# Kernel tuning notes

Measured on AMD Instinct MI355X. Metric: run time of the kernel, lower is better.

## Reference

```python
import jax, jax.numpy as jnp
import numpy as np

NUM_EXPERTS = 4
MLP_RATIO = 4


def setup_inputs() -> dict:
    key = jax.random.key(0)
    k1, k2, k3, k4, k5, k6 = jax.random.split(key, 6)
    B, N, D = 4, 4096, 1024
    OUT = 1024
    H = D * MLP_RATIO
    x = jax.random.normal(k1, (B, N, D), dtype=jnp.float32)
    expert_mask = jax.random.randint(k2, (B, N), 0, NUM_EXPERTS, dtype=jnp.int64)
    w1 = jax.random.normal(k3, (H, D), dtype=jnp.float32) * 0.02
    b1 = jax.random.normal(k4, (H,), dtype=jnp.float32) * 0.02
    w2 = jax.random.normal(k5, (OUT, H), dtype=jnp.float32) * 0.02
    b2 = jax.random.normal(k6, (OUT,), dtype=jnp.float32) * 0.02
    return {"x": x, "expert_mask": expert_mask, "w1": w1, "b1": b1, "w2": w2, "b2": b2}


def reference(x, expert_mask, w1, b1, w2, b2):
    # x: [B, N, D]; expert_mask: [B, N] in [0, NUM_EXPERTS)
    D = x.shape[-1]
    OUT = w2.shape[0]
    E = NUM_EXPERTS
    y = jnp.zeros(x.shape[:-1] + (OUT,), dtype=x.dtype)
    for e in range(E):
        shift = E - 1 - e  # expert E-1 uses full width
        d_in = D >> shift
        d_hid = d_in * MLP_RATIO
        d_out = OUT >> shift
        # nested slice of shared weights
        h = jax.nn.gelu(
            jnp.einsum('bnd,hd->bnh', x[..., :d_in], w1[:d_hid, :d_in]) + b1[:d_hid],
            approximate=False,
        )
        ye = jnp.einsum('bnh,oh->bno', h, w2[:d_out, :d_hid]) + b2[:d_out]
        ye = jnp.pad(ye, ((0, 0), (0, 0), (0, OUT - d_out)))  # zero-fill unused dims
        y = y + jnp.where((expert_mask == e)[..., None], ye, jnp.zeros((), dtype=x.dtype))
    return y
```

## Files before the change

kernel.cpp:

```cpp
#include <hip/hip_runtime.h>
#include <hip/hip_bf16.h>

#define T_TOK 16384
#define DMODEL 1024
#define HDIM 4096
#define OUTD 1024

typedef __attribute__((ext_vector_type(8))) short short8_t;
typedef __attribute__((ext_vector_type(4))) float f32x4;

#define WS_COUNTS_OFF 0
#define WS_LIST_OFF 128
#define WS_XC_OFF   ((size_t)1 << 20)
#define WS_W1BF_OFF ((size_t)34 << 20)
#define WS_W2BF_OFF ((size_t)43 << 20)
#define WS_HBUF_OFF ((size_t)52 << 20)

#define W1N (HDIM * DMODEL)
#define W2N (OUTD * HDIM)

__device__ __forceinline__ short f2bf(float f) {
    union { float f; unsigned u; } x; x.f = f;
    unsigned r = x.u + 0x7FFFu + ((x.u >> 16) & 1u);
    return (short)(r >> 16);
}

__device__ __forceinline__ float gelu_fast(float v) {
    float z = fabsf(v) * 0.7071067811865476f;
    float t = __builtin_amdgcn_rcpf(fmaf(0.3275911f, z, 1.0f));
    float poly = t * fmaf(t, fmaf(t, fmaf(t, fmaf(t, 1.061405429f, -1.453152027f),
                                          1.421413741f), -0.284496736f),
                          0.254829592f);
    float e = fmaf(-poly, __expf(-z * z), 1.0f);
    float erfv = copysignf(e, v);
    return 0.5f * v * (1.0f + erfv);
}

__device__ __forceinline__ void conv8(const float* __restrict__ s, short* __restrict__ d) {
    const float4* s4 = (const float4*)s;
    float4 f0 = s4[0], f1 = s4[1];
    short8_t v;
    v[0] = f2bf(f0.x); v[1] = f2bf(f0.y); v[2] = f2bf(f0.z); v[3] = f2bf(f0.w);
    v[4] = f2bf(f1.x); v[5] = f2bf(f1.y); v[6] = f2bf(f1.z); v[7] = f2bf(f1.w);
    *(short8_t*)d = v;
}

__device__ __forceinline__ void gl_lds16(const short* g, short* lds) {
    __builtin_amdgcn_global_load_lds(
        (const __attribute__((address_space(1))) void*)g,
        (__attribute__((address_space(3))) void*)lds, 16, 0, 0);
}

__device__ __forceinline__ void bases_for(const int* __restrict__ counts, int e,
                                          unsigned long long* hb,
                                          unsigned long long* xb) {
    unsigned long long h = 0, x = 0;
    for (int i = 0; i < e; ++i) {
        unsigned long long c = (unsigned long long)counts[i];
        int din = 128 << i;
        x += c * (unsigned long long)din;
        h += c * (unsigned long long)(din * 4);
    }
    *hb = h; *xb = x;
}

__global__ void k_convert(const float* __restrict__ w1, const float* __restrict__ w2,
                          short* __restrict__ w1bf, short* __restrict__ w2bf,
                          int* counts) {
    if (blockIdx.x == 0 && threadIdx.x < 4) counts[threadIdx.x] = 0;
    size_t elem = ((size_t)blockIdx.x * blockDim.x + threadIdx.x) * 8;
    if (elem < (size_t)W1N) {
        conv8(w1 + elem, w1bf + elem);
    } else {
        size_t o = elem - W1N; conv8(w2 + o, w2bf + o);
    }
}

__global__ void k_build(const int* __restrict__ mask, int* counts, int* list) {
    __shared__ int hcnt[4], hb[4], hpos[4];
    int tid = threadIdx.x;
    if (tid < 4) hcnt[tid] = 0;
    __syncthreads();
    int t = blockIdx.x * 256 + tid;
    int e = mask[t] & 3;
    atomicAdd(&hcnt[e], 1);
    __syncthreads();
    if (tid < 4) { hb[tid] = atomicAdd(&counts[tid], hcnt[tid]); hpos[tid] = 0; }
    __syncthreads();
    int p = atomicAdd(&hpos[e], 1);
    list[e * T_TOK + hb[e] + p] = t;
}

__global__ void k_xgather(const float* __restrict__ x, const int* __restrict__ counts,
                          const int* __restrict__ list, short* __restrict__ xc) {
    const int e = blockIdx.y;
    const int d_in = 128 << e;
    const int cnt = counts[e];
    unsigned long long hbD, xb;
    bases_for(counts, e, &hbD, &xb);
    const size_t nel = (size_t)cnt * d_in;
    const int* lst = list + e * T_TOK;
    short* dst = xc + xb;
    for (size_t idx = ((size_t)blockIdx.x * 256 + threadIdx.x) * 8; idx < nel;
         idx += (size_t)gridDim.x * 256 * 8) {
        int row = (int)(idx >> (7 + e));
        int col = (int)(idx & (d_in - 1));
        int tok = lst[row];
        conv8(x + (size_t)tok * DMODEL + col, dst + idx);
    }
}

__global__ __launch_bounds__(256) void k_pass1(
    const short* __restrict__ xc, const short* __restrict__ w1bf,
    const float* __restrict__ b1, const int* __restrict__ counts,
    short* __restrict__ hbuf)
{
    int by = blockIdx.y;
    int e, nt;
    if (by < 32)      { e = 3; nt = by; }
    else if (by < 48) { e = 2; nt = by - 32; }
    else if (by < 56) { e = 1; nt = by - 48; }
    else              { e = 0; nt = by - 56; }
    const int d_in = 128 << e;
    const int d_hid = d_in * 4;
    const int n0 = nt * 128;
    const int cnt = counts[e];
    unsigned long long hb, xb;
    bases_for(counts, e, &hb, &xb);
    const short* xe = xc + xb;

    __shared__ short Ab[64 * 64];
    __shared__ short Bb[128 * 64];

    const int tid = threadIdx.x;
    const int lane = tid & 63;
    const int w = tid >> 6;
    const int l3 = lane >> 3;
    const int ch = lane & 7;
    const int wm = (w & 1) * 32;
    const int wn = (w >> 1) * 64;

    for (int m0 = blockIdx.x * 64; m0 < cnt; m0 += 64 * 64) {
        int rA[2];
#pragma unroll
        for (int j = 0; j < 2; ++j) {
            int rr = m0 + j * 32 + w * 8 + l3;
            rA[j] = (rr >= cnt) ? (cnt - 1) : rr;
        }

        f32x4 acc[2][4];
#pragma unroll
        for (int i = 0; i < 2; ++i)
#pragma unroll
            for (int j = 0; j < 4; ++j)
                acc[i][j] = (f32x4){0.f, 0.f, 0.f, 0.f};

        for (int k0 = 0; k0 < d_in; k0 += 64) {
#pragma unroll
            for (int j = 0; j < 2; ++j) {
                int r = j * 32 + w * 8 + l3;
                gl_lds16(xe + (size_t)rA[j] * d_in + k0 + ((ch ^ (r & 7)) << 3),
                         &Ab[(j * 32 + w * 8) * 64]);
            }
#pragma unroll
            for (int j = 0; j < 4; ++j) {
                int r = j * 32 + w * 8 + l3;
                gl_lds16(w1bf + (size_t)(n0 + r) * DMODEL + k0 + ((ch ^ (r & 7)) << 3),
                         &Bb[(j * 32 + w * 8) * 64]);
            }
            __syncthreads();
#pragma unroll
            for (int kk = 0; kk < 2; ++kk) {
                short8_t af[2], bfr[4];
                const int q = (lane >> 4) + kk * 4;
#pragma unroll
                for (int mt = 0; mt < 2; ++mt) {
                    int row = wm + mt * 16 + (lane & 15);
                    af[mt] = *(const short8_t*)&Ab[((row << 3) | (q ^ (row & 7))) << 3];
                }
#pragma unroll
                for (int ntn = 0; ntn < 4; ++ntn) {
                    int row = wn + ntn * 16 + (lane & 15);
                    bfr[ntn] = *(const short8_t*)&Bb[((row << 3) | (q ^ (row & 7))) << 3];
                }
#pragma unroll
                for (int mt = 0; mt < 2; ++mt)
#pragma unroll
                    for (int ntn = 0; ntn < 4; ++ntn)
                        acc[mt][ntn] = __builtin_amdgcn_mfma_f32_16x16x32_bf16(
                            af[mt], bfr[ntn], acc[mt][ntn], 0, 0, 0);
            }
            __syncthreads();
        }

        const int cl = lane & 15;
        const int qr = lane >> 4;
#pragma unroll
        for (int ntn = 0; ntn < 4; ++ntn) {
            int col = n0 + wn + ntn * 16 + cl;
            float bias = b1[col];
#pragma unroll
            for (int mt = 0; mt < 2; ++mt) {
#pragma unroll
                for (int r = 0; r < 4; ++r) {
                    int row = wm + mt * 16 + qr * 4 + r;
                    if (m0 + row < cnt) {
                        float v = acc[mt][ntn][r] + bias;
                        hbuf[hb + (unsigned long long)(m0 + row) * d_hid + col] =
                            f2bf(gelu_fast(v));
                    }
                }
            }
        }
    }
}

__global__ __launch_bounds__(256) void k_pass2(
    const short* __restrict__ hbuf, const short* __restrict__ w2bf,
    const float* __restrict__ b2, const int* __restrict__ counts,
    const int* __restrict__ list, float* __restrict__ y)
{
    int by = blockIdx.y;
    if (by >= 15) {
        int e, nt;
        if (by < 19)      { e = 2; nt = by - 15 + 4; }
        else if (by < 25) { e = 1; nt = by - 19 + 2; }
        else              { e = 0; nt = by - 25 + 1; }
        const int cnt = counts[e];
        const int* lst = list + e * T_TOK;
        const int n0 = nt * 128;
        const int rt = threadIdx.x >> 2;
        const int cq = (threadIdx.x & 3) * 32;
        const float4 z4 = (float4){0.f, 0.f, 0.f, 0.f};
        for (int m0 = blockIdx.x * 64; m0 < cnt; m0 += gridDim.x * 64) {
            int row = m0 + rt;
            if (row < cnt) {
                float* dst = y + (size_t)lst[row] * OUTD + n0 + cq;
#pragma unroll
                for (int i = 0; i < 8; ++i) *(float4*)(dst + i * 4) = z4;
            }
        }
        return;
    }
    int e, nt;
    if (by < 8)       { e = 3; nt = by; }
    else if (by < 12) { e = 2; nt = by - 8; }
    else if (by < 14) { e = 1; nt = by - 12; }
    else              { e = 0; nt = 0; }
    const int d_in = 128 << e;
    const int d_hid = d_in * 4;
    const int n0 = nt * 128;
    const int cnt = counts[e];
    const int* lst = list + e * T_TOK;
    unsigned long long hb, xb;
    bases_for(counts, e, &hb, &xb);

    __shared__ short Ab[2 * 64 * 64];
    __shared__ short Bb[2 * 128 * 64];

    const int tid = threadIdx.x;
    const int lane = tid & 63;
    const int w = tid >> 6;
    const int l3 = lane >> 3;
    const int ch = lane & 7;
    const int wm = (w & 1) * 32;
    const int wn = (w >> 1) * 64;

#define P2_STAGE(kn, b) do {                                                   \
    _Pragma("unroll") for (int j = 0; j < 2; ++j) {                            \
        int r = j * 32 + w * 8 + l3;                                           \
        gl_lds16(hbuf + hb + (size_t)rA[j] * d_hid + (kn) + ((ch ^ (r & 7)) << 3), \
                 &Ab[(b) * 4096 + (j * 32 + w * 8) * 64]); }                   \
    _Pragma("unroll") for (int j = 0; j < 4; ++j) {                            \
        int r = j * 32 + w * 8 + l3;                                           \
        gl_lds16(w2bf + (size_t)(n0 + r) * HDIM + (kn) + ((ch ^ (r & 7)) << 3), \
                 &Bb[(b) * 8192 + (j * 32 + w * 8) * 64]); }                   \
} while (0)

    for (int m0 = blockIdx.x * 64; m0 < cnt; m0 += 64 * 64) {
        int rA[2];
#pragma unroll
        for (int j = 0; j < 2; ++j) {
            int rr = m0 + j * 32 + w * 8 + l3;
            rA[j] = (rr >= cnt) ? (cnt - 1) : rr;
        }

        f32x4 acc[2][4];
#pragma unroll
        for (int i = 0; i < 2; ++i)
#pragma unroll
            for (int j = 0; j < 4; ++j)
                acc[i][j] = (f32x4){0.f, 0.f, 0.f, 0.f};

        const int ks = d_hid >> 6;
        P2_STAGE(0, 0);
        for (int kt = 0; kt < ks; ++kt) {
            const int p = kt & 1;
            __builtin_amdgcn_s_barrier();
            if (kt + 1 < ks) {
                P2_STAGE((kt + 1) << 6, 1 - p);
                asm volatile("s_waitcnt vmcnt(6)" ::: "memory");
            } else {
                asm volatile("s_waitcnt vmcnt(0)" ::: "memory");
            }
            __builtin_amdgcn_s_barrier();
            const short* Ap = &Ab[p * 4096];
            const short* Bp = &Bb[p * 8192];
#pragma unroll
            for (int kk = 0; kk < 2; ++kk) {
                short8_t af[2], bfr[4];
                const int q = (lane >> 4) + kk * 4;
#pragma unroll
                for (int mt = 0; mt < 2; ++mt) {
                    int row = wm + mt * 16 + (lane & 15);
                    af[mt] = *(const short8_t*)&Ap[((row << 3) | (q ^ (row & 7))) << 3];
                }
#pragma unroll
                for (int ntn = 0; ntn < 4; ++ntn) {
                    int row = wn + ntn * 16 + (lane & 15);
                    bfr[ntn] = *(const short8_t*)&Bp[((row << 3) | (q ^ (row & 7))) << 3];
                }
#pragma unroll
                for (int mt = 0; mt < 2; ++mt)
#pragma unroll
                    for (int ntn = 0; ntn < 4; ++ntn)
                        acc[mt][ntn] = __builtin_amdgcn_mfma_f32_16x16x32_bf16(
                            af[mt], bfr[ntn], acc[mt][ntn], 0, 0, 0);
            }
        }

        const int cl = lane & 15;
        const int qr = lane >> 4;
#pragma unroll
        for (int ntn = 0; ntn < 4; ++ntn) {
            int col = n0 + wn + ntn * 16 + cl;
            float bias = b2[col];
#pragma unroll
            for (int mt = 0; mt < 2; ++mt) {
#pragma unroll
                for (int r = 0; r < 4; ++r) {
                    int row = wm + mt * 16 + qr * 4 + r;
                    if (m0 + row < cnt) {
                        int tok = lst[m0 + row];
                        y[(size_t)tok * OUTD + col] = acc[mt][ntn][r] + bias;
                    }
                }
            }
        }
    }
#undef P2_STAGE
}

extern "C" void kernel_launch(void* const* d_in, const int* in_sizes, int n_in,
                              void* d_out, int out_size, void* d_ws, size_t ws_size,
                              hipStream_t stream) {
    const float* x  = (const float*)d_in[0];
    const int* mask = (const int*)d_in[1];
    const float* w1 = (const float*)d_in[2];
    const float* b1 = (const float*)d_in[3];
    const float* w2 = (const float*)d_in[4];
    const float* b2 = (const float*)d_in[5];
    float* y = (float*)d_out;

    char* ws = (char*)d_ws;
    int* counts = (int*)(ws + WS_COUNTS_OFF);
    int* list = (int*)(ws + WS_LIST_OFF);
    short* xc   = (short*)(ws + WS_XC_OFF);
    short* w1bf = (short*)(ws + WS_W1BF_OFF);
    short* w2bf = (short*)(ws + WS_W2BF_OFF);
    short* hbuf = (short*)(ws + WS_HBUF_OFF);

    k_convert<<<(W1N + W2N) / 8 / 256, 256, 0, stream>>>(w1, w2, w1bf, w2bf, counts);
    k_build<<<T_TOK / 256, 256, 0, stream>>>(mask, counts, list);
    k_xgather<<<dim3(128, 4), 256, 0, stream>>>(x, counts, list, xc);
    k_pass1<<<dim3(64, 60), 256, 0, stream>>>(xc, w1bf, b1, counts, hbuf);
    k_pass2<<<dim3(64, 32), 256, 0, stream>>>(hbuf, w2bf, b2, counts, list, y);
}
```

Measured before the change: 367.0 us.

## Remap GEMM block indices so each XCD owns fixed weight column tiles

Both GEMM passes switch to a 1D grid and decode the block index so that blocks landing on the same XCD (blockIdx mod 8) share the same expert/N-tile. Weight tiles then stay resident in each XCD's private L2 instead of being fetched by every XCD. The zero-fill work in pass2 is also flattened into a balanced chunk list spread across 512 blocks rather than per-tile rows. Some launched blocks exit immediately, and the mapping depends on the round-robin XCD dispatch order.

```diff
diff --git a/kernel.cpp b/kernel.cpp
--- a/kernel.cpp
+++ b/kernel.cpp
@@ -115,12 +115,16 @@
     const float* __restrict__ b1, const int* __restrict__ counts,
     short* __restrict__ hbuf)
 {
-    int by = blockIdx.y;
+    const int d = blockIdx.x;
+    const int xcd = d & 7;
+    const int slot = d >> 3;
+    const int g = slot >> 6;
+    const int bx = slot & 63;
     int e, nt;
-    if (by < 32)      { e = 3; nt = by; }
-    else if (by < 48) { e = 2; nt = by - 32; }
-    else if (by < 56) { e = 1; nt = by - 48; }
-    else              { e = 0; nt = by - 56; }
+    if (g < 4)       { e = 3; nt = xcd * 4 + g; }
+    else if (g < 6)  { e = 2; nt = xcd * 2 + (g - 4); }
+    else if (g == 6) { e = 1; nt = xcd; }
+    else             { if (xcd >= 4) return; e = 0; nt = xcd; }
     const int d_in = 128 << e;
     const int d_hid = d_in * 4;
     const int n0 = nt * 128;
@@ -140,7 +144,7 @@
     const int wm = (w & 1) * 32;
     const int wn = (w >> 1) * 64;
 
-    for (int m0 = blockIdx.x * 64; m0 < cnt; m0 += 64 * 64) {
+    for (int m0 = bx * 64; m0 < cnt; m0 += 64 * 64) {
         int rA[2];
 #pragma unroll
         for (int j = 0; j < 2; ++j) {
@@ -220,22 +224,29 @@
     const float* __restrict__ b2, const int* __restrict__ counts,
     const int* __restrict__ list, float* __restrict__ y)
 {
-    int by = blockIdx.y;
-    if (by >= 15) {
-        int e, nt;
-        if (by < 19)      { e = 2; nt = by - 15 + 4; }
-        else if (by < 25) { e = 1; nt = by - 19 + 2; }
-        else              { e = 0; nt = by - 25 + 1; }
-        const int cnt = counts[e];
-        const int* lst = list + e * T_TOK;
-        const int n0 = nt * 128;
+    const int d = blockIdx.x;
+    const int xcd = d & 7;
+    const int slot = d >> 3;
+    const int g = slot >> 6;
+    const int bx = slot & 63;
+    if (g == 2) {
+        const int z = xcd * 64 + bx;
+        const int ch2 = (counts[2] + 63) >> 6, ch1 = (counts[1] + 63) >> 6,
+                  ch0 = (counts[0] + 63) >> 6;
+        const int n2 = ch2 * 4, n1 = ch1 * 6, n0c = ch0 * 7;
         const int rt = threadIdx.x >> 2;
         const int cq = (threadIdx.x & 3) * 32;
         const float4 z4 = (float4){0.f, 0.f, 0.f, 0.f};
-        for (int m0 = blockIdx.x * 64; m0 < cnt; m0 += gridDim.x * 64) {
-            int row = m0 + rt;
+        for (int c = z; c < n2 + n1 + n0c; c += 512) {
+            int e, nt, mi, cc = c;
+            if (cc < n2)            { e = 2; nt = 4 + cc / ch2; mi = cc % ch2; }
+            else { cc -= n2;
+                if (cc < n1)        { e = 1; nt = 2 + cc / ch1; mi = cc % ch1; }
+                else { cc -= n1;      e = 0; nt = 1 + cc / ch0; mi = cc % ch0; } }
+            const int cnt = counts[e];
+            int row = mi * 64 + rt;
             if (row < cnt) {
-                float* dst = y + (size_t)lst[row] * OUTD + n0 + cq;
+                float* dst = y + (size_t)list[e * T_TOK + row] * OUTD + nt * 128 + cq;
 #pragma unroll
                 for (int i = 0; i < 8; ++i) *(float4*)(dst + i * 4) = z4;
             }
@@ -243,10 +254,13 @@
         return;
     }
     int e, nt;
-    if (by < 8)       { e = 3; nt = by; }
-    else if (by < 12) { e = 2; nt = by - 8; }
-    else if (by < 14) { e = 1; nt = by - 12; }
-    else              { e = 0; nt = 0; }
+    if (g == 0) { e = 3; nt = xcd; }
+    else {
+        if (xcd < 4)       { e = 2; nt = xcd; }
+        else if (xcd < 6)  { e = 1; nt = xcd - 4; }
+        else if (xcd == 6) { e = 0; nt = 0; }
+        else return;
+    }
     const int d_in = 128 << e;
     const int d_hid = d_in * 4;
     const int n0 = nt * 128;
@@ -277,7 +291,7 @@
                  &Bb[(b) * 8192 + (j * 32 + w * 8) * 64]); }                   \
 } while (0)
 
-    for (int m0 = blockIdx.x * 64; m0 < cnt; m0 += 64 * 64) {
+    for (int m0 = bx * 64; m0 < cnt; m0 += 64 * 64) {
         int rA[2];
 #pragma unroll
         for (int j = 0; j < 2; ++j) {
@@ -373,6 +387,6 @@
     k_convert<<<(W1N + W2N) / 8 / 256, 256, 0, stream>>>(w1, w2, w1bf, w2bf, counts);
     k_build<<<T_TOK / 256, 256, 0, stream>>>(mask, counts, list);
     k_xgather<<<dim3(128, 4), 256, 0, stream>>>(x, counts, list, xc);
-    k_pass1<<<dim3(64, 60), 256, 0, stream>>>(xc, w1bf, b1, counts, hbuf);
-    k_pass2<<<dim3(64, 32), 256, 0, stream>>>(hbuf, w2bf, b2, counts, list, y);
-}
+    k_pass1<<<4096, 256, 0, stream>>>(xc, w1bf, b1, counts, hbuf);
+    k_pass2<<<1536, 256, 0, stream>>>(hbuf, w2bf, b2, counts, list, y);
+}
```

Result: faster. 359.0 us (-2.2%).
